# Optimization experiments

Hardware: AMD Instinct MI355X
Metric: run time of the kernel (lower is better)

Reference implementation:

```python
import jax, jax.numpy as jnp
import numpy as np

B, L, D = 2, 2048, 2048
N_HEADS, N_KV_HEADS, HEAD_DIM = 32, 8, 64
ROPE_BASE = 10000.0
SCALE = HEAD_DIM ** -0.5


def setup_inputs() -> dict:
    key = jax.random.key(0)
    k1, k2, k3 = jax.random.split(key, 3)
    op_size = N_HEADS * HEAD_DIM + 2 * N_KV_HEADS * HEAD_DIM  # 3072
    x = jax.random.normal(k1, (B, L, D), dtype=jnp.float32)
    Wqkv = jax.random.normal(k2, (op_size, D), dtype=jnp.float32) * (D ** -0.5)
    Wo = jax.random.normal(k3, (N_HEADS * HEAD_DIM, D), dtype=jnp.float32).T * (D ** -0.5)
    Wo = jnp.asarray(Wo)  # [D, n_heads*hd] stored torch-style as [out, in] = [D, D]
    return {"x": x, "Wqkv": Wqkv, "Wo": Wo}


def _rope(t, cos, sin):
    # non-traditional (half-split) RoPE: t is [B, H, L, hd]
    half = t.shape[-1] // 2
    t1, t2 = t[..., :half], t[..., half:]
    return jnp.concatenate([t1 * cos - t2 * sin, t2 * cos + t1 * sin], axis=-1)


def reference(x, Wqkv, Wo):
    b, l, d = x.shape
    qkv = jnp.einsum("bld,od->blo", x, Wqkv)  # fused QKV projection
    q_pos = N_HEADS * HEAD_DIM
    kv_pos = N_KV_HEADS * HEAD_DIM
    q = qkv[..., :q_pos].reshape(b, l, N_HEADS, HEAD_DIM).transpose(0, 2, 1, 3)
    k = qkv[..., q_pos:q_pos + kv_pos].reshape(b, l, N_KV_HEADS, HEAD_DIM).transpose(0, 2, 1, 3)
    v = qkv[..., q_pos + kv_pos:].reshape(b, l, N_KV_HEADS, HEAD_DIM).transpose(0, 2, 1, 3)

    # RoPE angles (offset=0, no cache)
    inv_freq = 1.0 / (ROPE_BASE ** (jnp.arange(0, HEAD_DIM, 2, dtype=jnp.float32) / HEAD_DIM))
    ang = jnp.arange(l, dtype=jnp.float32)[:, None] * inv_freq[None, :]  # [L, hd/2]
    cos, sin = jnp.cos(ang), jnp.sin(ang)  # broadcast over [B, H, L, hd/2]
    q = _rope(q, cos, sin)
    k = _rope(k, cos, sin)

    # GQA: expand kv heads to match query heads
    rep = N_HEADS // N_KV_HEADS
    k = jnp.repeat(k, rep, axis=1)
    v = jnp.repeat(v, rep, axis=1)

    scores = jnp.einsum("bhqd,bhkd->bhqk", q, k) * SCALE
    causal = jnp.tril(jnp.ones((l, l), dtype=bool))
    scores = jnp.where(causal, scores, jnp.finfo(scores.dtype).min)
    attn = jax.nn.softmax(scores, axis=-1)
    out = jnp.einsum("bhqk,bhkd->bhqd", attn, v)
    out = out.transpose(0, 2, 1, 3).reshape(b, l, N_HEADS * HEAD_DIM)
    return jnp.einsum("blh,dh->bld", out, Wo)
```

## Files before the change

### kernel.cpp

```cpp
#include <hip/hip_runtime.h>
#include <math.h>

#define B_   2
#define L_   2048
#define D_   2048
#define NH   32
#define NKV  8
#define HD   64
#define OP   3072
#define QPOS 2048
#define KPOS 2048
#define VPOS 2560
#define SCALE_ 0.125f
#define NEG_BIG -1.0e30f

typedef __attribute__((ext_vector_type(8))) short s16x8;
typedef __attribute__((ext_vector_type(4))) float f32x4;

__device__ __forceinline__ unsigned short f2bf(float f) {
  unsigned int u = __float_as_uint(f);
  u += 0x7fffu + ((u >> 16) & 1u);
  return (unsigned short)(u >> 16);
}
__device__ __forceinline__ float bf2f(unsigned short h) {
  return __uint_as_float((unsigned int)h << 16);
}

__device__ __forceinline__ void gload16(const unsigned short* g, unsigned short* l) {
  __builtin_amdgcn_global_load_lds(
      (const __attribute__((address_space(1))) unsigned int*)g,
      (__attribute__((address_space(3))) unsigned int*)l, 16, 0, 0);
}

__global__ __launch_bounds__(256)
void split3(const float* __restrict__ src, unsigned short* __restrict__ dst,
            int K, int mode) {
  const int r = blockIdx.x;
  const int c = threadIdx.x * 8;
  const float* s = src + (size_t)r * K + c;
  float4 v0 = *(const float4*)s;
  float4 v1 = *(const float4*)(s + 4);
  float v[8] = {v0.x, v0.y, v0.z, v0.w, v1.x, v1.y, v1.z, v1.w};
  unsigned short hi[8], lo[8];
#pragma unroll
  for (int j = 0; j < 8; ++j) {
    hi[j] = f2bf(v[j]);
    lo[j] = f2bf(v[j] - bf2f(hi[j]));
  }
  unsigned short* d = dst + (size_t)r * 3 * K;
  s16x8 hv, lv;
#pragma unroll
  for (int j = 0; j < 8; ++j) { hv[j] = (short)hi[j]; lv[j] = (short)lo[j]; }
  *(s16x8*)(d + c)         = hv;
  *(s16x8*)(d + K + c)     = (mode == 0) ? lv : hv;
  *(s16x8*)(d + 2 * K + c) = (mode == 0) ? hv : lv;
}

#define TBM 128
#define TBN 128
#define TBK 64

__global__ __launch_bounds__(256)
void gemm_bt_bf16(const unsigned short* __restrict__ A2,
                  const unsigned short* __restrict__ B2,
                  float* __restrict__ C, int M, int N, int K2) {
  __shared__ unsigned short As[TBM * TBK];
  __shared__ unsigned short Bs[TBN * TBK];

  const int t  = threadIdx.x;
  const int m0 = blockIdx.y * TBM;
  const int n0 = blockIdx.x * TBN;
  const int w  = t >> 6;
  const int l  = t & 63;
  const int wr = (w >> 1) * 64;
  const int wc = (w & 1) * 64;
  const int srow = t >> 3;
  const int scol = (t & 7) * 8;

  f32x4 acc[4][4];
#pragma unroll
  for (int m = 0; m < 4; ++m)
#pragma unroll
    for (int n = 0; n < 4; ++n)
#pragma unroll
      for (int q = 0; q < 4; ++q) acc[m][n][q] = 0.f;

  const int nsteps = K2 / TBK;
  for (int ks = 0; ks < nsteps; ++ks) {
    const size_t kb = (size_t)ks * TBK;
#pragma unroll
    for (int i = 0; i < 4; ++i) {
      int row = i * 32 + srow;
      gload16(A2 + (size_t)(m0 + row) * K2 + kb + scol, &As[row * TBK + scol]);
      gload16(B2 + (size_t)(n0 + row) * K2 + kb + scol, &Bs[row * TBK + scol]);
    }
    __syncthreads();

#pragma unroll
    for (int kk = 0; kk < 2; ++kk) {
      s16x8 af[4], bf[4];
      const int ko = kk * 32 + (l >> 4) * 8;
#pragma unroll
      for (int m = 0; m < 4; ++m)
        af[m] = *(const s16x8*)&As[(wr + m * 16 + (l & 15)) * TBK + ko];
#pragma unroll
      for (int n = 0; n < 4; ++n)
        bf[n] = *(const s16x8*)&Bs[(wc + n * 16 + (l & 15)) * TBK + ko];
#pragma unroll
      for (int m = 0; m < 4; ++m)
#pragma unroll
        for (int n = 0; n < 4; ++n)
          acc[m][n] = __builtin_amdgcn_mfma_f32_16x16x32_bf16(af[m], bf[n], acc[m][n], 0, 0, 0);
    }
    __syncthreads();
  }

#pragma unroll
  for (int m = 0; m < 4; ++m)
#pragma unroll
    for (int n = 0; n < 4; ++n) {
      int gr = m0 + wr + m * 16 + (l >> 4) * 4;
      int gc = n0 + wc + n * 16 + (l & 15);
#pragma unroll
      for (int j = 0; j < 4; ++j)
        C[(size_t)(gr + j) * N + gc] = acc[m][n][j];
    }
}

#define GBM 128
#define GBN 128
#define GBK 16
#define GPAD 4

__global__ __launch_bounds__(256)
void gemm_nt(const float* __restrict__ A, const float* __restrict__ Bm,
             float* __restrict__ C, int M, int N, int K) {
  __shared__ float Asf[GBK][GBM + GPAD];
  __shared__ float Bsf[GBK][GBN + GPAD];
  const int t  = threadIdx.x;
  const int m0 = blockIdx.y * GBM;
  const int n0 = blockIdx.x * GBN;
  const int tx = t & 15;
  const int ty = t >> 4;

  float acc[8][8];
#pragma unroll
  for (int i = 0; i < 8; ++i)
#pragma unroll
    for (int j = 0; j < 8; ++j) acc[i][j] = 0.f;

  for (int k0 = 0; k0 < K; k0 += GBK) {
#pragma unroll
    for (int i = 0; i < 2; ++i) {
      int f   = t + i * 256;
      int row = f >> 2;
      int kc  = (f & 3) << 2;
      float4 va = *(const float4*)(A + (size_t)(m0 + row) * K + k0 + kc);
      Asf[kc + 0][row] = va.x; Asf[kc + 1][row] = va.y;
      Asf[kc + 2][row] = va.z; Asf[kc + 3][row] = va.w;
      float4 vb = *(const float4*)(Bm + (size_t)(n0 + row) * K + k0 + kc);
      Bsf[kc + 0][row] = vb.x; Bsf[kc + 1][row] = vb.y;
      Bsf[kc + 2][row] = vb.z; Bsf[kc + 3][row] = vb.w;
    }
    __syncthreads();
#pragma unroll
    for (int kk = 0; kk < GBK; ++kk) {
      float a[8], b[8];
#pragma unroll
      for (int i = 0; i < 8; ++i) a[i] = Asf[kk][ty * 8 + i];
#pragma unroll
      for (int j = 0; j < 8; ++j) b[j] = Bsf[kk][tx * 8 + j];
#pragma unroll
      for (int i = 0; i < 8; ++i)
#pragma unroll
        for (int j = 0; j < 8; ++j) acc[i][j] += a[i] * b[j];
    }
    __syncthreads();
  }
#pragma unroll
  for (int i = 0; i < 8; ++i) {
    float* crow = C + (size_t)(m0 + ty * 8 + i) * N + n0 + tx * 8;
    *(float4*)(crow)     = make_float4(acc[i][0], acc[i][1], acc[i][2], acc[i][3]);
    *(float4*)(crow + 4) = make_float4(acc[i][4], acc[i][5], acc[i][6], acc[i][7]);
  }
}

__global__ void rope_tables(float* __restrict__ ctab, float* __restrict__ stab) {
  int idx = blockIdx.x * 256 + threadIdx.x;
  if (idx >= L_ * 32) return;
  int l = idx >> 5;
  int i = idx & 31;
  float freq = powf(10000.0f, -(float)(2 * i) / 64.0f);
  float ang  = (float)l * freq;
  ctab[idx] = cosf(ang);
  stab[idx] = sinf(ang);
}

__global__ __launch_bounds__(256)
void rope_inplace(float* __restrict__ qkv, const float* __restrict__ ctab,
                  const float* __restrict__ stab) {
  const int row = blockIdx.x;
  const int l   = row & (L_ - 1);
  float* p = qkv + (size_t)row * OP;
  const int t = threadIdx.x;
#pragma unroll
  for (int k = 0; k < 5; ++k) {
    int item = t + k * 256;
    int hh = item >> 5;
    int d  = item & 31;
    int off = (hh < NH) ? hh * HD + d : KPOS + (hh - NH) * HD + d;
    float sc = (hh < NH) ? SCALE_ : 1.0f;
    float c = ctab[l * 32 + d];
    float s = stab[l * 32 + d];
    float a = p[off];
    float bq = p[off + 32];
    p[off]      = (a * c - bq * s) * sc;
    p[off + 32] = (bq * c + a * s) * sc;
  }
}

#define CHUNK(row, kc) ((((row) >> 4) * 8 + (kc)) * 16 + ((row) & 15))

__global__ __launch_bounds__(256, 2)
void attn_fwd3(const float* __restrict__ qkv, float* __restrict__ out) {
  __shared__ __align__(16) unsigned short Kf[2][4096];
  __shared__ __align__(16) unsigned short Vf[2][4096];
  __shared__ __align__(16) unsigned short Sf[2][4096];

  const int t   = threadIdx.x;
  const int qt  = blockIdx.x;
  const int h   = blockIdx.y;
  const int b   = blockIdx.z;
  const int kvh = h >> 2;
  const int w   = t >> 6;
  const int l   = t & 63;
  const int r15 = l & 15;
  const int g   = l >> 4;
  const float* base = qkv + (size_t)b * L_ * OP;

  const int srow = t & 63;
  const int pb   = (t >> 6) * 2;

  s16x8 qhi[2], qlo[2];
  {
    const int qrow = qt * 64 + w * 16 + r15;
    const float* qsrc = base + (size_t)qrow * OP + h * HD + g * 8;
#pragma unroll
    for (int ks = 0; ks < 2; ++ks) {
      float4 a = *(const float4*)(qsrc + ks * 32);
      float4 c = *(const float4*)(qsrc + ks * 32 + 4);
      float v[8] = {a.x, a.y, a.z, a.w, c.x, c.y, c.z, c.w};
#pragma unroll
      for (int j = 0; j < 8; ++j) {
        unsigned short hh = f2bf(v[j]);
        qhi[ks][j] = (short)hh;
        qlo[ks][j] = (short)f2bf(v[j] - bf2f(hh));
      }
    }
  }

  f32x4 acco[4];
  float m_run[4], l_run[4];
#pragma unroll
  for (int m = 0; m < 4; ++m)
#pragma unroll
    for (int q = 0; q < 4; ++q) acco[m][q] = 0.f;
#pragma unroll
  for (int q = 0; q < 4; ++q) { m_run[q] = NEG_BIG; l_run[q] = 0.f; }

  for (int kt = 0; kt <= qt; ++kt) {
    {
      const float* gk = base + (size_t)(kt * 64 + srow) * OP + KPOS + kvh * HD + pb * 8;
      float kv[16];
#pragma unroll
      for (int i = 0; i < 4; ++i) {
        float4 u = *(const float4*)(gk + 4 * i);
        kv[4 * i] = u.x; kv[4 * i + 1] = u.y; kv[4 * i + 2] = u.z; kv[4 * i + 3] = u.w;
      }
      s16x8 h0, h1, l0, l1;
#pragma unroll
      for (int j = 0; j < 8; ++j) {
        unsigned short hh = f2bf(kv[j]);
        h0[j] = (short)hh; l0[j] = (short)f2bf(kv[j] - bf2f(hh));
        unsigned short h2 = f2bf(kv[j + 8]);
        h1[j] = (short)h2; l1[j] = (short)f2bf(kv[j + 8] - bf2f(h2));
      }
      *(s16x8*)&Kf[0][CHUNK(srow, pb) * 8]     = h0;
      *(s16x8*)&Kf[0][CHUNK(srow, pb + 1) * 8] = h1;
      *(s16x8*)&Kf[1][CHUNK(srow, pb) * 8]     = l0;
      *(s16x8*)&Kf[1][CHUNK(srow, pb + 1) * 8] = l1;
    }
    {
      const float* gv = base + (size_t)(kt * 64 + pb * 8) * OP + VPOS + kvh * HD + srow;
      s16x8 h0, h1, l0, l1;
#pragma unroll
      for (int kk = 0; kk < 8; ++kk) {
        float v0 = gv[(size_t)kk * OP];
        float v1 = gv[(size_t)(kk + 8) * OP];
        unsigned short hh = f2bf(v0);
        h0[kk] = (short)hh; l0[kk] = (short)f2bf(v0 - bf2f(hh));
        unsigned short h2 = f2bf(v1);
        h1[kk] = (short)h2; l1[kk] = (short)f2bf(v1 - bf2f(h2));
      }
      *(s16x8*)&Vf[0][CHUNK(srow, pb) * 8]     = h0;
      *(s16x8*)&Vf[0][CHUNK(srow, pb + 1) * 8] = h1;
      *(s16x8*)&Vf[1][CHUNK(srow, pb) * 8]     = l0;
      *(s16x8*)&Vf[1][CHUNK(srow, pb + 1) * 8] = l1;
    }
    __syncthreads();

    f32x4 accs[4];
#pragma unroll
    for (int n = 0; n < 4; ++n)
#pragma unroll
      for (int q = 0; q < 4; ++q) accs[n][q] = 0.f;

#pragma unroll
    for (int ks = 0; ks < 2; ++ks) {
      const int kc = ks * 4 + g;
#pragma unroll
      for (int n = 0; n < 4; ++n) {
        s16x8 bh = *(const s16x8*)&Kf[0][CHUNK(n * 16 + r15, kc) * 8];
        s16x8 bl = *(const s16x8*)&Kf[1][CHUNK(n * 16 + r15, kc) * 8];
        accs[n] = __builtin_amdgcn_mfma_f32_16x16x32_bf16(qhi[ks], bh, accs[n], 0, 0, 0);
        accs[n] = __builtin_amdgcn_mfma_f32_16x16x32_bf16(qlo[ks], bh, accs[n], 0, 0, 0);
        accs[n] = __builtin_amdgcn_mfma_f32_16x16x32_bf16(qhi[ks], bl, accs[n], 0, 0, 0);
      }
    }

    if (kt == qt) {
#pragma unroll
      for (int n = 0; n < 4; ++n) {
        int col = n * 16 + r15;
#pragma unroll
        for (int q = 0; q < 4; ++q) {
          int row = w * 16 + g * 4 + q;
          if (col > row) accs[n][q] = NEG_BIG;
        }
      }
    }

    float alpha[4];
#pragma unroll
    for (int q = 0; q < 4; ++q) {
      float mx = fmaxf(fmaxf(accs[0][q], accs[1][q]), fmaxf(accs[2][q], accs[3][q]));
      mx = fmaxf(mx, __shfl_xor(mx, 1));
      mx = fmaxf(mx, __shfl_xor(mx, 2));
      mx = fmaxf(mx, __shfl_xor(mx, 4));
      mx = fmaxf(mx, __shfl_xor(mx, 8));
      float mnew = fmaxf(m_run[q], mx);
      alpha[q] = __expf(m_run[q] - mnew);
      float ps = 0.f;
#pragma unroll
      for (int n = 0; n < 4; ++n) {
        float p = __expf(accs[n][q] - mnew);
        accs[n][q] = p;
        ps += p;
      }
      ps += __shfl_xor(ps, 1);
      ps += __shfl_xor(ps, 2);
      ps += __shfl_xor(ps, 4);
      ps += __shfl_xor(ps, 8);
      l_run[q] = l_run[q] * alpha[q] + ps;
      m_run[q] = mnew;
    }

#pragma unroll
    for (int n = 0; n < 4; ++n) {
      const int kc = n * 2 + (r15 >> 3);
#pragma unroll
      for (int q = 0; q < 4; ++q) {
        int e = CHUNK(w * 16 + g * 4 + q, kc) * 8 + (l & 7);
        float p = accs[n][q];
        unsigned short hh = f2bf(p);
        Sf[0][e] = hh;
        Sf[1][e] = f2bf(p - bf2f(hh));
      }
    }

    {
      int src = (r15 >> 2) << 4;
      float a0 = __shfl(alpha[0], src);
      float a1 = __shfl(alpha[1], src);
      float a2 = __shfl(alpha[2], src);
      float a3 = __shfl(alpha[3], src);
      int sel = r15 & 3;
      float aq = (sel == 0) ? a0 : (sel == 1) ? a1 : (sel == 2) ? a2 : a3;
#pragma unroll
      for (int m = 0; m < 4; ++m)
#pragma unroll
        for (int q = 0; q < 4; ++q) acco[m][q] *= aq;
    }

#pragma unroll
    for (int ks = 0; ks < 2; ++ks) {
      const int kc = ks * 4 + g;
      s16x8 bh = *(const s16x8*)&Sf[0][CHUNK(w * 16 + r15, kc) * 8];
      s16x8 bl = *(const s16x8*)&Sf[1][CHUNK(w * 16 + r15, kc) * 8];
#pragma unroll
      for (int m = 0; m < 4; ++m) {
        s16x8 ah = *(const s16x8*)&Vf[0][CHUNK(m * 16 + r15, kc) * 8];
        s16x8 al = *(const s16x8*)&Vf[1][CHUNK(m * 16 + r15, kc) * 8];
        acco[m] = __builtin_amdgcn_mfma_f32_16x16x32_bf16(ah, bh, acco[m], 0, 0, 0);
        acco[m] = __builtin_amdgcn_mfma_f32_16x16x32_bf16(al, bh, acco[m], 0, 0, 0);
        acco[m] = __builtin_amdgcn_mfma_f32_16x16x32_bf16(ah, bl, acco[m], 0, 0, 0);
      }
    }
    __syncthreads();
  }

  {
    int src = (r15 >> 2) << 4;
    float i0 = __shfl(1.f / l_run[0], src);
    float i1 = __shfl(1.f / l_run[1], src);
    float i2 = __shfl(1.f / l_run[2], src);
    float i3 = __shfl(1.f / l_run[3], src);
    int sel = r15 & 3;
    float invq = (sel == 0) ? i0 : (sel == 1) ? i1 : (sel == 2) ? i2 : i3;
    const int qrow = qt * 64 + w * 16 + r15;
    float* dst = out + (size_t)(b * L_ + qrow) * QPOS + h * HD + g * 4;
#pragma unroll
    for (int m = 0; m < 4; ++m) {
      *(float4*)(dst + m * 16) = make_float4(acco[m][0] * invq, acco[m][1] * invq,
                                             acco[m][2] * invq, acco[m][3] * invq);
    }
  }
}

extern "C" void kernel_launch(void* const* d_in, const int* in_sizes, int n_in,
                              void* d_out, int out_size, void* d_ws, size_t ws_size,
                              hipStream_t stream) {
  const float* x    = (const float*)d_in[0];
  const float* Wqkv = (const float*)d_in[1];
  const float* Wo   = (const float*)d_in[2];
  float* outp = (float*)d_out;
  float* ws   = (float*)d_ws;

  float* qkv_ws  = ws;
  float* attn_ws = qkv_ws + (size_t)(B_ * L_) * OP;
  float* ctab    = attn_ws + (size_t)(B_ * L_) * QPOS;
  float* stab    = ctab + (size_t)L_ * 32;
  unsigned short* A2 = (unsigned short*)(stab + (size_t)L_ * 32);
  unsigned short* B2 = A2 + (size_t)4096 * 6144;

  const size_t NEED = ((size_t)21102592) * 4 + ((size_t)44040192) * 2;
  const bool mfma_ok = ws_size >= NEED;

  if (mfma_ok) {
    split3<<<dim3(B_ * L_), 256, 0, stream>>>(x, A2, D_, 0);
    split3<<<dim3(OP), 256, 0, stream>>>(Wqkv, B2, D_, 1);
    gemm_bt_bf16<<<dim3(OP / TBN, (B_ * L_) / TBM), 256, 0, stream>>>(
        A2, B2, qkv_ws, B_ * L_, OP, 3 * D_);
  } else {
    gemm_nt<<<dim3(OP / GBN, (B_ * L_) / GBM), 256, 0, stream>>>(
        x, Wqkv, qkv_ws, B_ * L_, OP, D_);
  }

  rope_tables<<<dim3((L_ * 32 + 255) / 256), 256, 0, stream>>>(ctab, stab);
  rope_inplace<<<dim3(B_ * L_), 256, 0, stream>>>(qkv_ws, ctab, stab);

  dim3 ga(L_ / 64, NH, B_);
  attn_fwd3<<<ga, 256, 0, stream>>>(qkv_ws, attn_ws);

  if (mfma_ok) {
    split3<<<dim3(B_ * L_), 256, 0, stream>>>(attn_ws, A2, QPOS, 0);
    split3<<<dim3(D_), 256, 0, stream>>>(Wo, B2, QPOS, 1);
    gemm_bt_bf16<<<dim3(D_ / TBN, (B_ * L_) / TBM), 256, 0, stream>>>(
        A2, B2, outp, B_ * L_, D_, 3 * QPOS);
  } else {
    gemm_nt<<<dim3(D_ / GBN, (B_ * L_) / GBM), 256, 0, stream>>>(
        attn_ws, Wo, outp, B_ * L_, D_, QPOS);
  }
}
```

Before: 951.6 us.

## Pre-split K/V once and fuse bf16 split of attention output

```diff
diff --git a/kernel.cpp b/kernel.cpp
--- a/kernel.cpp
+++ b/kernel.cpp
@@ -15,6 +15,7 @@
 #define NEG_BIG -1.0e30f
 
 typedef __attribute__((ext_vector_type(8))) short s16x8;
+typedef __attribute__((ext_vector_type(4))) short s16x4;
 typedef __attribute__((ext_vector_type(4))) float f32x4;
 
 __device__ __forceinline__ unsigned short f2bf(float f) {
@@ -31,6 +32,8 @@
       (const __attribute__((address_space(1))) unsigned int*)g,
       (__attribute__((address_space(3))) unsigned int*)l, 16, 0, 0);
 }
+
+#define CHUNK(row, kc) ((((row) >> 4) * 8 + (kc)) * 16 + ((row) & 15))
 
 __global__ __launch_bounds__(256)
 void split3(const float* __restrict__ src, unsigned short* __restrict__ dst,
@@ -219,10 +222,63 @@
   }
 }
 
-#define CHUNK(row, kc) ((((row) >> 4) * 8 + (kc)) * 16 + ((row) & 15))
+__global__ __launch_bounds__(256)
+void split_kv(const float* __restrict__ qkv, unsigned short* __restrict__ Ksp,
+              unsigned short* __restrict__ Vsp) {
+  const int kt = blockIdx.x, kvh = blockIdx.y, b = blockIdx.z;
+  const int t = threadIdx.x;
+  const int srow = t & 63;
+  const int pb   = (t >> 6) * 2;
+  const size_t tb = (((size_t)(b * NKV + kvh) * 32) + kt) * 8192;
+  const float* base = qkv + (size_t)b * L_ * OP;
+
+  {
+    const float* gk = base + (size_t)(kt * 64 + srow) * OP + KPOS + kvh * HD + pb * 8;
+    float kv[16];
+#pragma unroll
+    for (int i = 0; i < 4; ++i) {
+      float4 u = *(const float4*)(gk + 4 * i);
+      kv[4 * i] = u.x; kv[4 * i + 1] = u.y; kv[4 * i + 2] = u.z; kv[4 * i + 3] = u.w;
+    }
+    s16x8 h0, h1, l0, l1;
+#pragma unroll
+    for (int j = 0; j < 8; ++j) {
+      unsigned short hh = f2bf(kv[j]);
+      h0[j] = (short)hh; l0[j] = (short)f2bf(kv[j] - bf2f(hh));
+      unsigned short h2 = f2bf(kv[j + 8]);
+      h1[j] = (short)h2; l1[j] = (short)f2bf(kv[j + 8] - bf2f(h2));
+    }
+    unsigned short* kd = Ksp + tb;
+    *(s16x8*)&kd[CHUNK(srow, pb) * 8]            = h0;
+    *(s16x8*)&kd[CHUNK(srow, pb + 1) * 8]        = h1;
+    *(s16x8*)&kd[4096 + CHUNK(srow, pb) * 8]     = l0;
+    *(s16x8*)&kd[4096 + CHUNK(srow, pb + 1) * 8] = l1;
+  }
+  {
+    const float* gv = base + (size_t)(kt * 64 + pb * 8) * OP + VPOS + kvh * HD + srow;
+    s16x8 h0, h1, l0, l1;
+#pragma unroll
+    for (int kk = 0; kk < 8; ++kk) {
+      float v0 = gv[(size_t)kk * OP];
+      float v1 = gv[(size_t)(kk + 8) * OP];
+      unsigned short hh = f2bf(v0);
+      h0[kk] = (short)hh; l0[kk] = (short)f2bf(v0 - bf2f(hh));
+      unsigned short h2 = f2bf(v1);
+      h1[kk] = (short)h2; l1[kk] = (short)f2bf(v1 - bf2f(h2));
+    }
+    unsigned short* vd = Vsp + tb;
+    *(s16x8*)&vd[CHUNK(srow, pb) * 8]            = h0;
+    *(s16x8*)&vd[CHUNK(srow, pb + 1) * 8]        = h1;
+    *(s16x8*)&vd[4096 + CHUNK(srow, pb) * 8]     = l0;
+    *(s16x8*)&vd[4096 + CHUNK(srow, pb + 1) * 8] = l1;
+  }
+}
 
 __global__ __launch_bounds__(256, 2)
-void attn_fwd3(const float* __restrict__ qkv, float* __restrict__ out) {
+void attn_fwd4(const float* __restrict__ qkv,
+               const unsigned short* __restrict__ Ksp,
+               const unsigned short* __restrict__ Vsp,
+               unsigned short* __restrict__ A2out) {
   __shared__ __align__(16) unsigned short Kf[2][4096];
   __shared__ __align__(16) unsigned short Vf[2][4096];
   __shared__ __align__(16) unsigned short Sf[2][4096];
@@ -238,9 +294,6 @@
   const int g   = l >> 4;
   const float* base = qkv + (size_t)b * L_ * OP;
 
-  const int srow = t & 63;
-  const int pb   = (t >> 6) * 2;
-
   s16x8 qhi[2], qlo[2];
   {
     const int qrow = qt * 64 + w * 16 + r15;
@@ -259,54 +312,34 @@
     }
   }
 
+  s16x8 onesf;
+#pragma unroll
+  for (int j = 0; j < 8; ++j) onesf[j] = (short)0x3F80;
+
   f32x4 acco[4];
-  float m_run[4], l_run[4];
+  f32x4 acc1;
+  float m_run[4];
 #pragma unroll
   for (int m = 0; m < 4; ++m)
 #pragma unroll
     for (int q = 0; q < 4; ++q) acco[m][q] = 0.f;
 #pragma unroll
-  for (int q = 0; q < 4; ++q) { m_run[q] = NEG_BIG; l_run[q] = 0.f; }
+  for (int q = 0; q < 4; ++q) acc1[q] = 0.f;
+#pragma unroll
+  for (int q = 0; q < 4; ++q) m_run[q] = NEG_BIG;
 
   for (int kt = 0; kt <= qt; ++kt) {
-    {
-      const float* gk = base + (size_t)(kt * 64 + srow) * OP + KPOS + kvh * HD + pb * 8;
-      float kv[16];
-#pragma unroll
-      for (int i = 0; i < 4; ++i) {
-        float4 u = *(const float4*)(gk + 4 * i);
-        kv[4 * i] = u.x; kv[4 * i + 1] = u.y; kv[4 * i + 2] = u.z; kv[4 * i + 3] = u.w;
-      }
-      s16x8 h0, h1, l0, l1;
-#pragma unroll
-      for (int j = 0; j < 8; ++j) {
-        unsigned short hh = f2bf(kv[j]);
-        h0[j] = (short)hh; l0[j] = (short)f2bf(kv[j] - bf2f(hh));
-        unsigned short h2 = f2bf(kv[j + 8]);
-        h1[j] = (short)h2; l1[j] = (short)f2bf(kv[j + 8] - bf2f(h2));
-      }
-      *(s16x8*)&Kf[0][CHUNK(srow, pb) * 8]     = h0;
-      *(s16x8*)&Kf[0][CHUNK(srow, pb + 1) * 8] = h1;
-      *(s16x8*)&Kf[1][CHUNK(srow, pb) * 8]     = l0;
-      *(s16x8*)&Kf[1][CHUNK(srow, pb + 1) * 8] = l1;
-    }
-    {
-      const float* gv = base + (size_t)(kt * 64 + pb * 8) * OP + VPOS + kvh * HD + srow;
-      s16x8 h0, h1, l0, l1;
-#pragma unroll
-      for (int kk = 0; kk < 8; ++kk) {
-        float v0 = gv[(size_t)kk * OP];
-        float v1 = gv[(size_t)(kk + 8) * OP];
-        unsigned short hh = f2bf(v0);
-        h0[kk] = (short)hh; l0[kk] = (short)f2bf(v0 - bf2f(hh));
-        unsigned short h2 = f2bf(v1);
-        h1[kk] = (short)h2; l1[kk] = (short)f2bf(v1 - bf2f(h2));
-      }
-      *(s16x8*)&Vf[0][CHUNK(srow, pb) * 8]     = h0;
-      *(s16x8*)&Vf[0][CHUNK(srow, pb + 1) * 8] = h1;
-      *(s16x8*)&Vf[1][CHUNK(srow, pb) * 8]     = l0;
-      *(s16x8*)&Vf[1][CHUNK(srow, pb + 1) * 8] = l1;
-    }
+    const size_t tb = (((size_t)(b * NKV + kvh) * 32) + kt) * 8192;
+    const unsigned short* kt_k = Ksp + tb;
+    const unsigned short* kt_v = Vsp + tb;
+#pragma unroll
+    for (int p = 0; p < 2; ++p)
+#pragma unroll
+      for (int i = 0; i < 2; ++i) {
+        const int e = (i * 256 + t) * 8;
+        gload16(kt_k + p * 4096 + e, &Kf[p][e]);
+        gload16(kt_v + p * 4096 + e, &Vf[p][e]);
+      }
     __syncthreads();
 
     f32x4 accs[4];
@@ -350,19 +383,9 @@
       mx = fmaxf(mx, __shfl_xor(mx, 8));
       float mnew = fmaxf(m_run[q], mx);
       alpha[q] = __expf(m_run[q] - mnew);
-      float ps = 0.f;
-#pragma unroll
-      for (int n = 0; n < 4; ++n) {
-        float p = __expf(accs[n][q] - mnew);
-        accs[n][q] = p;
-        ps += p;
-      }
-      ps += __shfl_xor(ps, 1);
-      ps += __shfl_xor(ps, 2);
-      ps += __shfl_xor(ps, 4);
-      ps += __shfl_xor(ps, 8);
-      l_run[q] = l_run[q] * alpha[q] + ps;
       m_run[q] = mnew;
+#pragma unroll
+      for (int n = 0; n < 4; ++n) accs[n][q] = __expf(accs[n][q] - mnew);
     }
 
 #pragma unroll
@@ -390,6 +413,8 @@
       for (int m = 0; m < 4; ++m)
 #pragma unroll
         for (int q = 0; q < 4; ++q) acco[m][q] *= aq;
+#pragma unroll
+      for (int q = 0; q < 4; ++q) acc1[q] *= aq;
     }
 
 #pragma unroll
@@ -397,6 +422,8 @@
       const int kc = ks * 4 + g;
       s16x8 bh = *(const s16x8*)&Sf[0][CHUNK(w * 16 + r15, kc) * 8];
       s16x8 bl = *(const s16x8*)&Sf[1][CHUNK(w * 16 + r15, kc) * 8];
+      acc1 = __builtin_amdgcn_mfma_f32_16x16x32_bf16(onesf, bh, acc1, 0, 0, 0);
+      acc1 = __builtin_amdgcn_mfma_f32_16x16x32_bf16(onesf, bl, acc1, 0, 0, 0);
 #pragma unroll
       for (int m = 0; m < 4; ++m) {
         s16x8 ah = *(const s16x8*)&Vf[0][CHUNK(m * 16 + r15, kc) * 8];
@@ -410,20 +437,159 @@
   }
 
   {
-    int src = (r15 >> 2) << 4;
-    float i0 = __shfl(1.f / l_run[0], src);
-    float i1 = __shfl(1.f / l_run[1], src);
-    float i2 = __shfl(1.f / l_run[2], src);
-    float i3 = __shfl(1.f / l_run[3], src);
-    int sel = r15 & 3;
-    float invq = (sel == 0) ? i0 : (sel == 1) ? i1 : (sel == 2) ? i2 : i3;
+    float invq = 1.f / acc1[0];
     const int qrow = qt * 64 + w * 16 + r15;
-    float* dst = out + (size_t)(b * L_ + qrow) * QPOS + h * HD + g * 4;
+    unsigned short* arow = A2out + (size_t)(b * L_ + qrow) * (3 * QPOS) + h * HD + g * 4;
 #pragma unroll
     for (int m = 0; m < 4; ++m) {
-      *(float4*)(dst + m * 16) = make_float4(acco[m][0] * invq, acco[m][1] * invq,
-                                             acco[m][2] * invq, acco[m][3] * invq);
-    }
+      s16x4 hv, lv;
+#pragma unroll
+      for (int j = 0; j < 4; ++j) {
+        float v = acco[m][j] * invq;
+        unsigned short hh = f2bf(v);
+        hv[j] = (short)hh;
+        lv[j] = (short)f2bf(v - bf2f(hh));
+      }
+      *(s16x4*)(arow + m * 16)            = hv;
+      *(s16x4*)(arow + QPOS + m * 16)     = lv;
+      *(s16x4*)(arow + 2 * QPOS + m * 16) = hv;
+    }
+  }
+}
+
+#define LDA 68
+
+__global__ __launch_bounds__(256)
+void attn_fwd2(const float* __restrict__ qkv, float* __restrict__ out) {
+  __shared__ float QsT[HD][LDA];
+  __shared__ float KsT[HD][LDA];
+  __shared__ float Vs[64][LDA];
+  __shared__ float SsT[64][LDA];
+
+  const int t   = threadIdx.x;
+  const int qt  = blockIdx.x;
+  const int h   = blockIdx.y;
+  const int b   = blockIdx.z;
+  const int kvh = h >> 2;
+  const int tx  = t & 15;
+  const int ty  = t >> 4;
+  const int r   = t >> 2;
+  const int seg = t & 3;
+  const float* base = qkv + (size_t)b * L_ * OP;
+
+  {
+    const float* src = base + (size_t)(qt * 64 + r) * OP + h * HD + seg * 16;
+#pragma unroll
+    for (int u = 0; u < 4; ++u) {
+      float4 v = *(const float4*)(src + 4 * u);
+      int d = seg * 16 + 4 * u;
+      QsT[d + 0][r] = v.x; QsT[d + 1][r] = v.y;
+      QsT[d + 2][r] = v.z; QsT[d + 3][r] = v.w;
+    }
+  }
+
+  float m_run[4], l_run[4], o[4][4];
+#pragma unroll
+  for (int i = 0; i < 4; ++i) {
+    m_run[i] = NEG_BIG; l_run[i] = 0.f;
+#pragma unroll
+    for (int j = 0; j < 4; ++j) o[i][j] = 0.f;
+  }
+
+  for (int kt = 0; kt <= qt; ++kt) {
+    {
+      const float* ksrc = base + (size_t)(kt * 64 + r) * OP + KPOS + kvh * HD + seg * 16;
+      const float* vsrc = base + (size_t)(kt * 64 + r) * OP + VPOS + kvh * HD + seg * 16;
+#pragma unroll
+      for (int u = 0; u < 4; ++u) {
+        float4 kv = *(const float4*)(ksrc + 4 * u);
+        int d = seg * 16 + 4 * u;
+        KsT[d + 0][r] = kv.x; KsT[d + 1][r] = kv.y;
+        KsT[d + 2][r] = kv.z; KsT[d + 3][r] = kv.w;
+        *(float4*)&Vs[r][seg * 16 + 4 * u] = *(const float4*)(vsrc + 4 * u);
+      }
+    }
+    __syncthreads();
+
+    float s4[4][4];
+#pragma unroll
+    for (int i = 0; i < 4; ++i)
+#pragma unroll
+      for (int j = 0; j < 4; ++j) s4[i][j] = 0.f;
+
+#pragma unroll 4
+    for (int d = 0; d < 64; ++d) {
+      float4 qa = *(const float4*)&QsT[d][ty * 4];
+      float4 kb = *(const float4*)&KsT[d][tx * 4];
+      float a[4] = {qa.x, qa.y, qa.z, qa.w};
+      float bb[4] = {kb.x, kb.y, kb.z, kb.w};
+#pragma unroll
+      for (int i = 0; i < 4; ++i)
+#pragma unroll
+        for (int j = 0; j < 4; ++j) s4[i][j] += a[i] * bb[j];
+    }
+
+    if (kt == qt) {
+#pragma unroll
+      for (int i = 0; i < 4; ++i)
+#pragma unroll
+        for (int j = 0; j < 4; ++j)
+          if (tx * 4 + j > ty * 4 + i) s4[i][j] = NEG_BIG;
+    }
+
+#pragma unroll
+    for (int i = 0; i < 4; ++i) {
+      float mloc = fmaxf(fmaxf(s4[i][0], s4[i][1]), fmaxf(s4[i][2], s4[i][3]));
+      mloc = fmaxf(mloc, __shfl_xor(mloc, 1));
+      mloc = fmaxf(mloc, __shfl_xor(mloc, 2));
+      mloc = fmaxf(mloc, __shfl_xor(mloc, 4));
+      mloc = fmaxf(mloc, __shfl_xor(mloc, 8));
+      float mnew  = fmaxf(m_run[i], mloc);
+      float alpha = __expf(m_run[i] - mnew);
+      float psum  = 0.f;
+#pragma unroll
+      for (int j = 0; j < 4; ++j) {
+        float pv = __expf(s4[i][j] - mnew);
+        s4[i][j] = pv;
+        psum += pv;
+      }
+      psum += __shfl_xor(psum, 1);
+      psum += __shfl_xor(psum, 2);
+      psum += __shfl_xor(psum, 4);
+      psum += __shfl_xor(psum, 8);
+      l_run[i] = l_run[i] * alpha + psum;
+      m_run[i] = mnew;
+#pragma unroll
+      for (int j = 0; j < 4; ++j) o[i][j] *= alpha;
+    }
+
+#pragma unroll
+    for (int j = 0; j < 4; ++j)
+#pragma unroll
+      for (int i = 0; i < 4; ++i)
+        SsT[tx * 4 + j][ty * 4 + i] = s4[i][j];
+    __syncthreads();
+
+#pragma unroll 4
+    for (int k = 0; k < 64; ++k) {
+      float4 pa = *(const float4*)&SsT[k][ty * 4];
+      float4 vb = *(const float4*)&Vs[k][tx * 4];
+      float a[4] = {pa.x, pa.y, pa.z, pa.w};
+      float bb[4] = {vb.x, vb.y, vb.z, vb.w};
+#pragma unroll
+      for (int i = 0; i < 4; ++i)
+#pragma unroll
+        for (int j = 0; j < 4; ++j) o[i][j] += a[i] * bb[j];
+    }
+    __syncthreads();
+  }
+
+#pragma unroll
+  for (int i = 0; i < 4; ++i) {
+    float inv = 1.f / l_run[i];
+    float* dst = out + ((size_t)(b * L_ + qt * 64 + ty * 4 + i)) * QPOS + h * HD + tx * 4;
+    *(float4*)dst = make_float4(o[i][0] * inv, o[i][1] * inv,
+                                o[i][2] * inv, o[i][3] * inv);
   }
 }
 
@@ -443,6 +609,9 @@
   unsigned short* A2 = (unsigned short*)(stab + (size_t)L_ * 32);
   unsigned short* B2 = A2 + (size_t)4096 * 6144;
 
+  unsigned short* Ksp = (unsigned short*)attn_ws;
+  unsigned short* Vsp = Ksp + (size_t)B_ * NKV * 32 * 8192;
+
   const size_t NEED = ((size_t)21102592) * 4 + ((size_t)44040192) * 2;
   const bool mfma_ok = ws_size >= NEED;
 
@@ -451,23 +620,22 @@
     split3<<<dim3(OP), 256, 0, stream>>>(Wqkv, B2, D_, 1);
     gemm_bt_bf16<<<dim3(OP / TBN, (B_ * L_) / TBM), 256, 0, stream>>>(
         A2, B2, qkv_ws, B_ * L_, OP, 3 * D_);
-  } else {
-    gemm_nt<<<dim3(OP / GBN, (B_ * L_) / GBM), 256, 0, stream>>>(
-        x, Wqkv, qkv_ws, B_ * L_, OP, D_);
-  }
-
-  rope_tables<<<dim3((L_ * 32 + 255) / 256), 256, 0, stream>>>(ctab, stab);
-  rope_inplace<<<dim3(B_ * L_), 256, 0, stream>>>(qkv_ws, ctab, stab);
-
-  dim3 ga(L_ / 64, NH, B_);
-  attn_fwd3<<<ga, 256, 0, stream>>>(qkv_ws, attn_ws);
-
-  if (mfma_ok) {
-    split3<<<dim3(B_ * L_), 256, 0, stream>>>(attn_ws, A2, QPOS, 0);
+
+    rope_tables<<<dim3((L_ * 32 + 255) / 256), 256, 0, stream>>>(ctab, stab);
+    rope_inplace<<<dim3(B_ * L_), 256, 0, stream>>>(qkv_ws, ctab, stab);
+
+    split_kv<<<dim3(32, NKV, B_), 256, 0, stream>>>(qkv_ws, Ksp, Vsp);
+    attn_fwd4<<<dim3(L_ / 64, NH, B_), 256, 0, stream>>>(qkv_ws, Ksp, Vsp, A2);
+
     split3<<<dim3(D_), 256, 0, stream>>>(Wo, B2, QPOS, 1);
     gemm_bt_bf16<<<dim3(D_ / TBN, (B_ * L_) / TBM), 256, 0, stream>>>(
         A2, B2, outp, B_ * L_, D_, 3 * QPOS);
   } else {
+    gemm_nt<<<dim3(OP / GBN, (B_ * L_) / GBM), 256, 0, stream>>>(
+        x, Wqkv, qkv_ws, B_ * L_, OP, D_);
+    rope_tables<<<dim3((L_ * 32 + 255) / 256), 256, 0, stream>>>(ctab, stab);
+    rope_inplace<<<dim3(B_ * L_), 256, 0, stream>>>(qkv_ws, ctab, stab);
+    attn_fwd2<<<dim3(L_ / 64, NH, B_), 256, 0, stream>>>(qkv_ws, attn_ws);
     gemm_nt<<<dim3(D_ / GBN, (B_ * L_) / GBM), 256, 0, stream>>>(
         attn_ws, Wo, outp, B_ * L_, D_, QPOS);
   }
```

Result: faster. 826.7 us (-13.1%).
